# Performance work log

Measured on AMD Instinct MI355X. Metric: run time of the kernel, lower is better.

The kernel has to match this reference:

```python
import jax, jax.numpy as jnp
import numpy as np

NUM_HEADS = 16

def _rms_norm(x):
    # F.rms_norm over last dim, eps = dtype machine epsilon (torch default eps=None)
    eps = jnp.finfo(jnp.float32).eps
    ms = jnp.mean(jnp.square(x.astype(jnp.float32)), axis=-1, keepdims=True)
    return (x.astype(jnp.float32) * jax.lax.rsqrt(ms + eps)).astype(x.dtype)

def _rotary_tables(T, head_dim):
    # inv_freq = (1/1024)**linspace(0,1,head_dim//4), padded with zeros to head_dim//2
    quarter = head_dim // 4
    inv_freq = (1.0 / 1024.0) ** jnp.linspace(0.0, 1.0, quarter, dtype=jnp.float32)
    inv_freq = jnp.concatenate([inv_freq, jnp.zeros(quarter, dtype=jnp.float32)])
    t = jnp.arange(T, dtype=jnp.float32)
    theta = t[:, None] * inv_freq[None, :]          # [T, head_dim//2]
    return jnp.cos(theta), jnp.sin(theta)

def _rotary(x, cos, sin):
    # x: [B, T, H, hd]; rotate in fp32, cast back
    xf = x.astype(jnp.float32)
    x1, x2 = jnp.split(xf, 2, axis=-1)
    c = cos[None, :, None, :]
    s = sin[None, :, None, :]
    y1 = x1 * c + x2 * s
    y2 = -x1 * s + x2 * c
    return jnp.concatenate([y1, y2], axis=-1).astype(x.dtype)

def setup_inputs() -> dict:
    key = jax.random.key(0)
    ks = jax.random.split(key, 7)
    B, T, D = 1, 2048, 1024
    sc = 1.0 / np.sqrt(D)
    return {
        "x": jax.random.normal(ks[0], (B, T, D), jnp.float32),
        "vi": jax.random.normal(ks[1], (B, T, D), jnp.float32),
        "Wq": jax.random.normal(ks[2], (D, D), jnp.float32) * sc,
        "Wk": jax.random.normal(ks[3], (D, D), jnp.float32) * sc,
        "Wv": jax.random.normal(ks[4], (D, D), jnp.float32) * sc,
        "Wproj": jax.random.normal(ks[5], (D, D), jnp.float32) * sc,
        "lambdas": jnp.array([0.5, 0.5], jnp.float32),
    }

def reference(x, vi, Wq, Wk, Wv, Wproj, lambdas):
    B, T, D = x.shape
    H = NUM_HEADS
    hd = D // H
    q = (x @ Wq.T).reshape(B, T, H, hd)
    k = (x @ Wk.T).reshape(B, T, H, hd)
    v = (x @ Wv.T).reshape(B, T, H, hd)
    # value residual: lambda-mixed v
    v = lambdas[0] * v + lambdas[1] * vi.reshape(B, T, H, hd)
    q, k = _rms_norm(q), _rms_norm(k)
    cos, sin = _rotary_tables(T, hd)
    q, k = _rotary(q, cos, sin), _rotary(k, cos, sin)
    # causal attention, default flex_attention scale = 1/sqrt(head_dim)
    scores = jnp.einsum('bthd,bshd->bhts', q, k) / jnp.sqrt(jnp.float32(hd))
    causal = jnp.tril(jnp.ones((T, T), dtype=bool))
    scores = jnp.where(causal[None, None], scores, jnp.float32(-1e30))
    attn = jax.nn.softmax(scores, axis=-1)
    y = jnp.einsum('bhts,bshd->bthd', attn, v).reshape(B, T, D)
    return y @ Wproj.T
```

## Files before the change

### kernel.cpp

```cpp
#include <hip/hip_runtime.h>
#include <math.h>

#define T_SEQ 2048
#define D_MODEL 1024
#define NH 16
#define HD 64

typedef unsigned short ushort_t;
typedef unsigned int uint_t;
typedef short short8 __attribute__((ext_vector_type(8)));
typedef float floatx4 __attribute__((ext_vector_type(4)));

__device__ __forceinline__ ushort_t f2bf(float f) {
    uint_t u = __float_as_uint(f);
    u += 0x7FFFu + ((u >> 16) & 1u);
    return (ushort_t)(u >> 16);
}
__device__ __forceinline__ uint_t pack2(float a, float b) {
    return (uint_t)f2bf(a) | ((uint_t)f2bf(b) << 16);
}
__device__ __forceinline__ void cp16(ushort_t* dst, const ushort_t* src) {
    uint4 a = ((const uint4*)src)[0];
    uint4 b = ((const uint4*)src)[1];
    ((uint4*)dst)[0] = a;
    ((uint4*)dst)[1] = b;
}
__device__ __forceinline__ void gload16(const ushort_t* g, ushort_t* l) {
    __builtin_amdgcn_global_load_lds(
        (const __attribute__((address_space(1))) void*)g,
        (__attribute__((address_space(3))) void*)l, 16, 0, 0);
}

#define LDK 72

__global__ __launch_bounds__(256) void to_bf16(
        const float* __restrict__ x,  const float* __restrict__ wq,
        const float* __restrict__ wk, const float* __restrict__ wv,
        const float* __restrict__ wp,
        ushort_t* __restrict__ xb,  ushort_t* __restrict__ wqb,
        ushort_t* __restrict__ wkb, ushort_t* __restrict__ wvb,
        ushort_t* __restrict__ wpb)
{
    size_t i = (size_t)blockIdx.x * 256 + threadIdx.x;
    const float* src; ushort_t* dst; size_t off;
    if (i < 262144)      { src = x;  dst = xb;  off = i; }
    else if (i < 393216) { src = wq; dst = wqb; off = i - 262144; }
    else if (i < 524288) { src = wk; dst = wkb; off = i - 393216; }
    else if (i < 655360) { src = wv; dst = wvb; off = i - 524288; }
    else                 { src = wp; dst = wpb; off = i - 655360; }
    float4 f0 = ((const float4*)src)[off * 2];
    float4 f1 = ((const float4*)src)[off * 2 + 1];
    uint4 u;
    u.x = pack2(f0.x, f0.y); u.y = pack2(f0.z, f0.w);
    u.z = pack2(f1.x, f1.y); u.w = pack2(f1.z, f1.w);
    ((uint4*)dst)[off] = u;
}

__global__ __launch_bounds__(256) void gemm_qkv(
        const ushort_t* __restrict__ xb,
        const ushort_t* __restrict__ Wqb, const ushort_t* __restrict__ Wkb,
        const ushort_t* __restrict__ Wvb,
        const float* __restrict__ vi, const float* __restrict__ lam,
        ushort_t* __restrict__ qb, ushort_t* __restrict__ kb,
        ushort_t* __restrict__ vbt)
{
    const int z = blockIdx.z;
    const ushort_t* __restrict__ W = (z == 0) ? Wqb : (z == 1) ? Wkb : Wvb;
    const int row0 = blockIdx.y * 64;
    const int col0 = blockIdx.x * 128;

    __shared__ ushort_t As[2 * 64 * 64];
    __shared__ ushort_t Bs[2 * 128 * 64];

    const int tid = threadIdx.x;
    const int wave = tid >> 6, lane = tid & 63;
    const int wm = wave >> 1, wn = wave & 1;
    const int l15 = lane & 15, quad = lane >> 4;
    const int srow  = tid >> 3;
    const int sslot = (tid & 7) ^ (srow & 7);

    floatx4 acc[2][4];
    #pragma unroll
    for (int i = 0; i < 2; ++i)
        #pragma unroll
        for (int j = 0; j < 4; ++j)
            acc[i][j] = (floatx4){0.f, 0.f, 0.f, 0.f};

    auto stageAB = [&](int k0, int p) {
        ushort_t* Ap = As + p * 4096;
        ushort_t* Bp = Bs + p * 8192;
        #pragma unroll
        for (int c = 0; c < 2; ++c)
            gload16(xb + (size_t)(row0 + c * 32 + srow) * D_MODEL + k0 + sslot * 8,
                    Ap + c * 2048 + tid * 8);
        #pragma unroll
        for (int c = 0; c < 4; ++c)
            gload16(W + (size_t)(col0 + c * 32 + srow) * D_MODEL + k0 + sslot * 8,
                    Bp + c * 2048 + tid * 8);
    };

    stageAB(0, 0);
    int cur = 0;
    for (int k0 = 0; k0 < D_MODEL; k0 += 64) {
        asm volatile("s_waitcnt vmcnt(0)" ::: "memory");
        __builtin_amdgcn_s_barrier();
        const ushort_t* Ac = As + cur * 4096;
        const ushort_t* Bc = Bs + cur * 8192;
        short8 a[2][2], b[2][4];
        #pragma unroll
        for (int kh = 0; kh < 2; ++kh) {
            const int slot = ((kh * 4 + quad) ^ (l15 & 7)) << 3;
            #pragma unroll
            for (int i = 0; i < 2; ++i)
                a[kh][i] = *(const short8*)(Ac + (32 * wm + i * 16 + l15) * 64 + slot);
            #pragma unroll
            for (int j = 0; j < 4; ++j)
                b[kh][j] = *(const short8*)(Bc + (64 * wn + j * 16 + l15) * 64 + slot);
        }
        __builtin_amdgcn_sched_barrier(0);
        if (k0 + 64 < D_MODEL) stageAB(k0 + 64, cur ^ 1);
        __builtin_amdgcn_sched_barrier(0);
        #pragma unroll
        for (int kh = 0; kh < 2; ++kh)
            #pragma unroll
            for (int i = 0; i < 2; ++i)
                #pragma unroll
                for (int j = 0; j < 4; ++j)
                    acc[i][j] = __builtin_amdgcn_mfma_f32_16x16x32_bf16(a[kh][i], b[kh][j], acc[i][j], 0, 0, 0);
        cur ^= 1;
    }

    if (z < 2) {
        ushort_t* __restrict__ o = (z == 0) ? qb : kb;
        const float oscale = (z == 0) ? 0.125f : 1.0f;
        const int hbase = col0 + 64 * wn;
        const float eps = 1.1920929e-7f;
        const float fr = exp2f(-10.0f * (float)l15 / 15.0f);
        #pragma unroll
        for (int i = 0; i < 2; ++i)
            #pragma unroll
            for (int r = 0; r < 4; ++r) {
                const int t = row0 + 32 * wm + i * 16 + quad * 4 + r;
                float v0 = acc[i][0][r], v1 = acc[i][1][r];
                float v2 = acc[i][2][r], v3 = acc[i][3][r];
                float ss = v0 * v0 + v1 * v1 + v2 * v2 + v3 * v3;
                ss += __shfl_xor(ss, 1);
                ss += __shfl_xor(ss, 2);
                ss += __shfl_xor(ss, 4);
                ss += __shfl_xor(ss, 8);
                const float sc = rsqrtf(ss * (1.0f / 64.0f) + eps);
                v0 *= sc; v1 *= sc; v2 *= sc; v3 *= sc;
                const float th = (float)t * fr;
                const float cs = cosf(th), sn = sinf(th);
                const float y0 = v0 * cs + v2 * sn;
                const float y2 = v2 * cs - v0 * sn;
                const size_t rb = (size_t)t * D_MODEL + hbase;
                o[rb +  0 + l15] = f2bf(y0 * oscale);
                o[rb + 16 + l15] = f2bf(v1 * oscale);
                o[rb + 32 + l15] = f2bf(y2 * oscale);
                o[rb + 48 + l15] = f2bf(v3 * oscale);
            }
    } else {
        const float l0 = lam[0], l1 = lam[1];
        #pragma unroll
        for (int i = 0; i < 2; ++i)
            #pragma unroll
            for (int j = 0; j < 4; ++j) {
                const int tb = row0 + 32 * wm + i * 16 + quad * 4;
                const int jj = col0 + 64 * wn + j * 16 + l15;
                float b0 = l0 * acc[i][j][0] + l1 * vi[(size_t)(tb + 0) * D_MODEL + jj];
                float b1 = l0 * acc[i][j][1] + l1 * vi[(size_t)(tb + 1) * D_MODEL + jj];
                float b2 = l0 * acc[i][j][2] + l1 * vi[(size_t)(tb + 2) * D_MODEL + jj];
                float b3 = l0 * acc[i][j][3] + l1 * vi[(size_t)(tb + 3) * D_MODEL + jj];
                uint2 u;
                u.x = pack2(b0, b1);
                u.y = pack2(b2, b3);
                *(uint2*)(vbt + (size_t)jj * T_SEQ + tb) = u;
            }
    }
}

__global__ __launch_bounds__(256) void attn(
        const ushort_t* __restrict__ qb, const ushort_t* __restrict__ kb,
        const ushort_t* __restrict__ vbt, ushort_t* __restrict__ yb,
        float* __restrict__ Opart, float* __restrict__ Lpart)
{
    const int h = blockIdx.x;
    const int x = blockIdx.y;
    int qt, ct_begin, ct_end, pidx;
    if (x < 28) {
        qt = 27 - (x >> 1);
        const int w = qt + 1;
        const int c0 = (w + 1) >> 1;
        if ((x & 1) == 0) { ct_begin = 0;  ct_end = c0; }
        else              { ct_begin = c0; ct_end = w;  }
        pidx = h * 40 + 12 + (qt - 14) * 2 + (x & 1);
    } else if (x < 40) {
        const int xx = x - 28;
        qt = 28 + xx / 3;
        const int c = xx % 3;
        const int w = qt + 1;
        const int b0 = (w + 2) / 3;
        const int b1 = (2 * w + 2) / 3;
        ct_begin = (c == 0) ? 0  : (c == 1) ? b0 : b1;
        ct_end   = (c == 0) ? b0 : (c == 1) ? b1 : w;
        pidx = h * 40 + (qt - 28) * 3 + c;
    } else {
        qt = 53 - x;
        ct_begin = 0; ct_end = qt + 1;
        pidx = -1;
    }
    const int t0 = qt * 64;

    __shared__ ushort_t Ks[2 * 64 * 64];
    __shared__ ushort_t Vs[2 * 64 * 64];
    __shared__ ushort_t QPs[64 * LDK];

    const int tid = threadIdx.x;
    const int wave = tid >> 6, lane = tid & 63;
    const int l15 = lane & 15, quad = lane >> 4;
    const int r4 = tid >> 2, c4 = (tid & 3) * 16;
    const int srow  = tid >> 3;
    const int sslot = (tid & 7) ^ (srow & 7);
    const int bx = l15 & 7;

    cp16(QPs + r4 * LDK + c4, qb + (size_t)(t0 + r4) * D_MODEL + h * HD + c4);
    __syncthreads();
    short8 qf[2];
    qf[0] = *(const short8*)(QPs + (16 * wave + l15) * LDK + 0  + quad * 8);
    qf[1] = *(const short8*)(QPs + (16 * wave + l15) * LDK + 32 + quad * 8);

    auto stageKV = [&](int kt, int p) {
        const int s0 = kt * 64;
        ushort_t* Kp = Ks + p * 4096;
        ushort_t* Vp = Vs + p * 4096;
        gload16(kb  + (size_t)(s0 + srow)      * D_MODEL + h * HD + sslot * 8, Kp + tid * 8);
        gload16(kb  + (size_t)(s0 + 32 + srow) * D_MODEL + h * HD + sslot * 8, Kp + 2048 + tid * 8);
        gload16(vbt + (size_t)(h * HD + srow)      * T_SEQ + s0 + sslot * 8,   Vp + tid * 8);
        gload16(vbt + (size_t)(h * HD + 32 + srow) * T_SEQ + s0 + sslot * 8,   Vp + 2048 + tid * 8);
    };

    float l_acc[4];
    floatx4 O[4];
    #pragma unroll
    for (int r = 0; r < 4; ++r) l_acc[r] = 0.0f;
    #pragma unroll
    for (int d = 0; d < 4; ++d) O[d] = (floatx4){0.f, 0.f, 0.f, 0.f};

    stageKV(ct_begin, 0);
    int cur = 0;
    for (int kt = ct_begin; kt < ct_end; ++kt) {
        const bool haveNext = (kt + 1 < ct_end);
        if (haveNext) {
            stageKV(kt + 1, cur ^ 1);
            asm volatile("s_waitcnt vmcnt(4)" ::: "memory");
        } else {
            asm volatile("s_waitcnt vmcnt(0)" ::: "memory");
        }
        __builtin_amdgcn_s_barrier();

        const ushort_t* Kc = Ks + cur * 4096;
        const ushort_t* Vc = Vs + cur * 4096;

        floatx4 sa[4];
        #pragma unroll
        for (int ct = 0; ct < 4; ++ct) {
            const ushort_t* krow = Kc + (ct * 16 + l15) * 64;
            short8 b0 = *(const short8*)(krow + ((quad ^ bx) << 3));
            short8 b1 = *(const short8*)(krow + (((quad + 4) ^ bx) << 3));
            floatx4 t4 = (floatx4){0.f, 0.f, 0.f, 0.f};
            t4 = __builtin_amdgcn_mfma_f32_16x16x32_bf16(qf[0], b0, t4, 0, 0, 0);
            t4 = __builtin_amdgcn_mfma_f32_16x16x32_bf16(qf[1], b1, t4, 0, 0, 0);
            sa[ct] = t4;
        }
        if (kt == qt) {
            #pragma unroll
            for (int ct = 0; ct < 4; ++ct)
                #pragma unroll
                for (int r = 0; r < 4; ++r) {
                    int trow = 16 * wave + quad * 4 + r;
                    int scol = ct * 16 + l15;
                    if (scol > trow) sa[ct][r] = -1e30f;
                }
        }
        float p[4][4];
        #pragma unroll
        for (int ct = 0; ct < 4; ++ct)
            #pragma unroll
            for (int r = 0; r < 4; ++r) {
                p[ct][r] = __expf(sa[ct][r] - 8.0f);
                l_acc[r] += p[ct][r];
            }

        #pragma unroll
        for (int ct = 0; ct < 4; ++ct)
            #pragma unroll
            for (int r = 0; r < 4; ++r)
                QPs[(16 * wave + quad * 4 + r) * LDK + ct * 16 + l15] = f2bf(p[ct][r]);

        short8 pa0 = *(const short8*)(QPs + (16 * wave + l15) * LDK + 0  + quad * 8);
        short8 pa1 = *(const short8*)(QPs + (16 * wave + l15) * LDK + 32 + quad * 8);
        #pragma unroll
        for (int dt = 0; dt < 4; ++dt) {
            const ushort_t* vrow = Vc + (dt * 16 + l15) * 64;
            short8 vb0 = *(const short8*)(vrow + ((quad ^ bx) << 3));
            short8 vb1 = *(const short8*)(vrow + (((quad + 4) ^ bx) << 3));
            O[dt] = __builtin_amdgcn_mfma_f32_16x16x32_bf16(pa0, vb0, O[dt], 0, 0, 0);
            O[dt] = __builtin_amdgcn_mfma_f32_16x16x32_bf16(pa1, vb1, O[dt], 0, 0, 0);
        }

        asm volatile("" ::: "memory");
        __builtin_amdgcn_s_barrier();
        cur ^= 1;
    }

    float l_run[4];
    #pragma unroll
    for (int r = 0; r < 4; ++r) {
        float s = l_acc[r];
        s += __shfl_xor(s, 1);
        s += __shfl_xor(s, 2);
        s += __shfl_xor(s, 4);
        s += __shfl_xor(s, 8);
        l_run[r] = s;
    }

    if (pidx < 0) {
        #pragma unroll
        for (int r = 0; r < 4; ++r) {
            const float inv_l = 1.0f / l_run[r];
            const int t = t0 + 16 * wave + quad * 4 + r;
            #pragma unroll
            for (int dt = 0; dt < 4; ++dt)
                yb[(size_t)t * D_MODEL + h * HD + dt * 16 + l15] = f2bf(O[dt][r] * inv_l);
        }
    } else {
        float* __restrict__ Op = Opart + (size_t)pidx * 4096;
        #pragma unroll
        for (int r = 0; r < 4; ++r) {
            const int row = 16 * wave + quad * 4 + r;
            #pragma unroll
            for (int dt = 0; dt < 4; ++dt)
                Op[row * 64 + dt * 16 + l15] = O[dt][r];
            if (l15 == 0) Lpart[(size_t)pidx * 64 + row] = l_run[r];
        }
    }
}

__global__ __launch_bounds__(256) void attn_combine(
        const float* __restrict__ Opart, const float* __restrict__ Lpart,
        ushort_t* __restrict__ yb)
{
    const int h  = blockIdx.x;
    const int qt = 14 + (int)blockIdx.y;
    const int tid = threadIdx.x;
    const int row  = tid >> 2;
    const int dseg = (tid & 3) * 16;
    int s0, nc;
    if (qt >= 28) { s0 = (qt - 28) * 3;        nc = 3; }
    else          { s0 = 12 + (qt - 14) * 2;   nc = 2; }
    const int p0 = h * 40 + s0;

    float accv[16];
    #pragma unroll
    for (int e = 0; e < 16; ++e) accv[e] = 0.0f;
    float lsum = 0.0f;
    for (int c = 0; c < nc; ++c) {
        const float* Op = Opart + (size_t)(p0 + c) * 4096 + row * 64 + dseg;
        lsum += Lpart[(size_t)(p0 + c) * 64 + row];
        #pragma unroll
        for (int g = 0; g < 4; ++g) {
            float4 a = ((const float4*)Op)[g];
            accv[g * 4 + 0] += a.x;
            accv[g * 4 + 1] += a.y;
            accv[g * 4 + 2] += a.z;
            accv[g * 4 + 3] += a.w;
        }
    }
    const float inv = 1.0f / lsum;

    uint_t u[8];
    #pragma unroll
    for (int g = 0; g < 4; ++g) {
        u[g * 2 + 0] = pack2(accv[g * 4 + 0] * inv, accv[g * 4 + 1] * inv);
        u[g * 2 + 1] = pack2(accv[g * 4 + 2] * inv, accv[g * 4 + 3] * inv);
    }
    const int t = qt * 64 + row;
    uint4* dst = (uint4*)(yb + (size_t)t * D_MODEL + h * HD + dseg);
    dst[0] = make_uint4(u[0], u[1], u[2], u[3]);
    dst[1] = make_uint4(u[4], u[5], u[6], u[7]);
}

__global__ __launch_bounds__(256) void gemm_proj(
        const ushort_t* __restrict__ yb, const ushort_t* __restrict__ Wpb,
        float* __restrict__ out)
{
    const int row0 = blockIdx.y * 64;
    const int col0 = blockIdx.x * 128;

    __shared__ ushort_t As[2 * 64 * 64];
    __shared__ ushort_t Bs[2 * 128 * 64];

    const int tid = threadIdx.x;
    const int wave = tid >> 6, lane = tid & 63;
    const int wm = wave >> 1, wn = wave & 1;
    const int l15 = lane & 15, quad = lane >> 4;
    const int srow  = tid >> 3;
    const int sslot = (tid & 7) ^ (srow & 7);

    floatx4 acc[2][4];
    #pragma unroll
    for (int i = 0; i < 2; ++i)
        #pragma unroll
        for (int j = 0; j < 4; ++j)
            acc[i][j] = (floatx4){0.f, 0.f, 0.f, 0.f};

    auto stageAB = [&](int k0, int p) {
        ushort_t* Ap = As + p * 4096;
        ushort_t* Bp = Bs + p * 8192;
        #pragma unroll
        for (int c = 0; c < 2; ++c)
            gload16(yb + (size_t)(row0 + c * 32 + srow) * D_MODEL + k0 + sslot * 8,
                    Ap + c * 2048 + tid * 8);
        #pragma unroll
        for (int c = 0; c < 4; ++c)
            gload16(Wpb + (size_t)(col0 + c * 32 + srow) * D_MODEL + k0 + sslot * 8,
                    Bp + c * 2048 + tid * 8);
    };

    stageAB(0, 0);
    int cur = 0;
    for (int k0 = 0; k0 < D_MODEL; k0 += 64) {
        asm volatile("s_waitcnt vmcnt(0)" ::: "memory");
        __builtin_amdgcn_s_barrier();
        const ushort_t* Ac = As + cur * 4096;
        const ushort_t* Bc = Bs + cur * 8192;
        short8 a[2][2], b[2][4];
        #pragma unroll
        for (int kh = 0; kh < 2; ++kh) {
            const int slot = ((kh * 4 + quad) ^ (l15 & 7)) << 3;
            #pragma unroll
            for (int i = 0; i < 2; ++i)
                a[kh][i] = *(const short8*)(Ac + (32 * wm + i * 16 + l15) * 64 + slot);
            #pragma unroll
            for (int j = 0; j < 4; ++j)
                b[kh][j] = *(const short8*)(Bc + (64 * wn + j * 16 + l15) * 64 + slot);
        }
        __builtin_amdgcn_sched_barrier(0);
        if (k0 + 64 < D_MODEL) stageAB(k0 + 64, cur ^ 1);
        __builtin_amdgcn_sched_barrier(0);
        #pragma unroll
        for (int kh = 0; kh < 2; ++kh)
            #pragma unroll
            for (int i = 0; i < 2; ++i)
                #pragma unroll
                for (int j = 0; j < 4; ++j)
                    acc[i][j] = __builtin_amdgcn_mfma_f32_16x16x32_bf16(a[kh][i], b[kh][j], acc[i][j], 0, 0, 0);
        cur ^= 1;
    }

    #pragma unroll
    for (int i = 0; i < 2; ++i)
        #pragma unroll
        for (int j = 0; j < 4; ++j) {
            const int t = row0 + 32 * wm + i * 16 + quad * 4;
            const int jj = col0 + 64 * wn + j * 16 + l15;
            #pragma unroll
            for (int r = 0; r < 4; ++r)
                out[(size_t)(t + r) * D_MODEL + jj] = acc[i][j][r];
        }
}

extern "C" void kernel_launch(void* const* d_in, const int* in_sizes, int n_in,
                              void* d_out, int out_size, void* d_ws, size_t ws_size,
                              hipStream_t stream) {
    (void)in_sizes; (void)n_in; (void)out_size; (void)ws_size;
    const float* x   = (const float*)d_in[0];
    const float* vi  = (const float*)d_in[1];
    const float* Wq  = (const float*)d_in[2];
    const float* Wk  = (const float*)d_in[3];
    const float* Wv  = (const float*)d_in[4];
    const float* Wp  = (const float*)d_in[5];
    const float* lam = (const float*)d_in[6];

    char* base = (char*)d_ws;
    ushort_t* xb  = (ushort_t*)(base);
    ushort_t* wqb = (ushort_t*)(base + (size_t)4  * 1048576);
    ushort_t* wkb = (ushort_t*)(base + (size_t)6  * 1048576);
    ushort_t* wvb = (ushort_t*)(base + (size_t)8  * 1048576);
    ushort_t* wpb = (ushort_t*)(base + (size_t)10 * 1048576);
    ushort_t* qb  = (ushort_t*)(base + (size_t)12 * 1048576);
    ushort_t* kb  = (ushort_t*)(base + (size_t)16 * 1048576);
    ushort_t* vbt = (ushort_t*)(base + (size_t)20 * 1048576);
    ushort_t* yb  = (ushort_t*)(base + (size_t)24 * 1048576);
    float* Opart  = (float*)(base);
    float* Lpart  = (float*)d_out;
    float* out = (float*)d_out;

    to_bf16<<<dim3(786432 / 256), 256, 0, stream>>>(x, Wq, Wk, Wv, Wp, xb, wqb, wkb, wvb, wpb);
    gemm_qkv<<<dim3(8, 32, 3), 256, 0, stream>>>(xb, wqb, wkb, wvb, vi, lam, qb, kb, vbt);
    attn<<<dim3(16, 54), 256, 0, stream>>>(qb, kb, vbt, yb, Opart, Lpart);
    attn_combine<<<dim3(16, 18), 256, 0, stream>>>(Opart, Lpart, yb);
    gemm_proj<<<dim3(8, 32), 256, 0, stream>>>(yb, wpb, out);
}
```

Measured before the change: 144.2 us.

## Reschedule KV prefetch after QK MFMAs, drop trailing barrier, swizzle QP tile

Result: no change. 142.5 us (-1.2%).

```diff
diff --git a/kernel.cpp b/kernel.cpp
--- a/kernel.cpp
+++ b/kernel.cpp
@@ -19,19 +19,11 @@
 __device__ __forceinline__ uint_t pack2(float a, float b) {
     return (uint_t)f2bf(a) | ((uint_t)f2bf(b) << 16);
 }
-__device__ __forceinline__ void cp16(ushort_t* dst, const ushort_t* src) {
-    uint4 a = ((const uint4*)src)[0];
-    uint4 b = ((const uint4*)src)[1];
-    ((uint4*)dst)[0] = a;
-    ((uint4*)dst)[1] = b;
-}
 __device__ __forceinline__ void gload16(const ushort_t* g, ushort_t* l) {
     __builtin_amdgcn_global_load_lds(
         (const __attribute__((address_space(1))) void*)g,
         (__attribute__((address_space(3))) void*)l, 16, 0, 0);
 }
-
-#define LDK 72
 
 __global__ __launch_bounds__(256) void to_bf16(
         const float* __restrict__ x,  const float* __restrict__ wq,
@@ -214,21 +206,30 @@
 
     __shared__ ushort_t Ks[2 * 64 * 64];
     __shared__ ushort_t Vs[2 * 64 * 64];
-    __shared__ ushort_t QPs[64 * LDK];
+    __shared__ ushort_t QPs[64 * 64];
 
     const int tid = threadIdx.x;
     const int wave = tid >> 6, lane = tid & 63;
     const int l15 = lane & 15, quad = lane >> 4;
-    const int r4 = tid >> 2, c4 = (tid & 3) * 16;
     const int srow  = tid >> 3;
     const int sslot = (tid & 7) ^ (srow & 7);
     const int bx = l15 & 7;
 
-    cp16(QPs + r4 * LDK + c4, qb + (size_t)(t0 + r4) * D_MODEL + h * HD + c4);
+    {
+        const int r4 = tid >> 2, c4 = (tid & 3) * 16;
+        const ushort_t* src = qb + (size_t)(t0 + r4) * D_MODEL + h * HD + c4;
+        uint4 A = ((const uint4*)src)[0];
+        uint4 B = ((const uint4*)src)[1];
+        const int rs = r4 & 7;
+        const int s0 = (c4 >> 3) ^ rs;
+        const int s1 = ((c4 >> 3) + 1) ^ rs;
+        *(uint4*)(QPs + r4 * 64 + s0 * 8) = A;
+        *(uint4*)(QPs + r4 * 64 + s1 * 8) = B;
+    }
     __syncthreads();
     short8 qf[2];
-    qf[0] = *(const short8*)(QPs + (16 * wave + l15) * LDK + 0  + quad * 8);
-    qf[1] = *(const short8*)(QPs + (16 * wave + l15) * LDK + 32 + quad * 8);
+    qf[0] = *(const short8*)(QPs + (16 * wave + l15) * 64 + ((quad ^ bx) << 3));
+    qf[1] = *(const short8*)(QPs + (16 * wave + l15) * 64 + (((quad + 4) ^ bx) << 3));
 
     auto stageKV = [&](int kt, int p) {
         const int s0 = kt * 64;
@@ -250,19 +251,14 @@
     stageKV(ct_begin, 0);
     int cur = 0;
     for (int kt = ct_begin; kt < ct_end; ++kt) {
-        const bool haveNext = (kt + 1 < ct_end);
-        if (haveNext) {
-            stageKV(kt + 1, cur ^ 1);
-            asm volatile("s_waitcnt vmcnt(4)" ::: "memory");
-        } else {
-            asm volatile("s_waitcnt vmcnt(0)" ::: "memory");
-        }
+        asm volatile("s_waitcnt vmcnt(0)" ::: "memory");
         __builtin_amdgcn_s_barrier();
 
         const ushort_t* Kc = Ks + cur * 4096;
         const ushort_t* Vc = Vs + cur * 4096;
 
         floatx4 sa[4];
+        __builtin_amdgcn_s_setprio(1);
         #pragma unroll
         for (int ct = 0; ct < 4; ++ct) {
             const ushort_t* krow = Kc + (ct * 16 + l15) * 64;
@@ -273,6 +269,11 @@
             t4 = __builtin_amdgcn_mfma_f32_16x16x32_bf16(qf[1], b1, t4, 0, 0, 0);
             sa[ct] = t4;
         }
+        __builtin_amdgcn_s_setprio(0);
+        __builtin_amdgcn_sched_barrier(0);
+        if (kt + 1 < ct_end) stageKV(kt + 1, cur ^ 1);
+        __builtin_amdgcn_sched_barrier(0);
+
         if (kt == qt) {
             #pragma unroll
             for (int ct = 0; ct < 4; ++ct)
@@ -295,11 +296,15 @@
         #pragma unroll
         for (int ct = 0; ct < 4; ++ct)
             #pragma unroll
-            for (int r = 0; r < 4; ++r)
-                QPs[(16 * wave + quad * 4 + r) * LDK + ct * 16 + l15] = f2bf(p[ct][r]);
-
-        short8 pa0 = *(const short8*)(QPs + (16 * wave + l15) * LDK + 0  + quad * 8);
-        short8 pa1 = *(const short8*)(QPs + (16 * wave + l15) * LDK + 32 + quad * 8);
+            for (int r = 0; r < 4; ++r) {
+                const int row = 16 * wave + quad * 4 + r;
+                const int ps = (ct * 2 + (l15 >> 3)) ^ (row & 7);
+                QPs[row * 64 + ps * 8 + (l15 & 7)] = f2bf(p[ct][r]);
+            }
+
+        short8 pa0 = *(const short8*)(QPs + (16 * wave + l15) * 64 + ((quad ^ bx) << 3));
+        short8 pa1 = *(const short8*)(QPs + (16 * wave + l15) * 64 + (((quad + 4) ^ bx) << 3));
+        __builtin_amdgcn_s_setprio(1);
         #pragma unroll
         for (int dt = 0; dt < 4; ++dt) {
             const ushort_t* vrow = Vc + (dt * 16 + l15) * 64;
@@ -308,9 +313,7 @@
             O[dt] = __builtin_amdgcn_mfma_f32_16x16x32_bf16(pa0, vb0, O[dt], 0, 0, 0);
             O[dt] = __builtin_amdgcn_mfma_f32_16x16x32_bf16(pa1, vb1, O[dt], 0, 0, 0);
         }
-
-        asm volatile("" ::: "memory");
-        __builtin_amdgcn_s_barrier();
+        __builtin_amdgcn_s_setprio(0);
         cur ^= 1;
     }
 
```
